# Kernel tuning notes

Hardware: AMD Instinct MI355X
Metric: run time of the kernel (lower is better)

## Reference

```python
import jax, jax.numpy as jnp
import numpy as np

N = 100000
E = 1600000
D = 128
EPS = 1e-5


def setup_inputs() -> dict:
    key = jax.random.key(0)
    ks = jax.random.split(key, 6)
    X = jax.random.normal(ks[0], (N, D), dtype=jnp.float32)
    edge_weight = jax.random.uniform(ks[1], (E,), dtype=jnp.float32)
    W = jax.random.normal(ks[2], (2 * D, D), dtype=jnp.float32) * (1.0 / np.sqrt(2 * D))
    b = jax.random.normal(ks[3], (D,), dtype=jnp.float32) * 0.01
    gamma = jnp.ones((D,), dtype=jnp.float32)
    beta = jnp.zeros((D,), dtype=jnp.float32)
    edge_src = jax.random.randint(ks[4], (E,), 0, N, dtype=jnp.int32)
    edge_dst = jax.random.randint(ks[5], (E,), 0, N, dtype=jnp.int32)
    return {"X": X, "edge_weight": edge_weight, "W": W, "b": b,
            "gamma": gamma, "beta": beta,
            "edge_src": edge_src, "edge_dst": edge_dst}


def reference(X, edge_weight, W, b, gamma, beta, edge_src, edge_dst):
    # Pre-LayerNorm over feature dim
    mu = jnp.mean(X, axis=-1, keepdims=True)
    var = jnp.mean(jnp.square(X - mu), axis=-1, keepdims=True)
    H = (X - mu) * jax.lax.rsqrt(var + EPS) * gamma + beta
    # dropout is identity in eval mode
    # sparse neighbor aggregation: neigh[i] = sum_{e: dst[e]=i} w[e] * H[src[e]]
    msgs = edge_weight[:, None] * H[edge_src]          # [E, D]
    neigh = jax.ops.segment_sum(msgs, edge_dst, num_segments=X.shape[0])  # [N, D]
    cat = jnp.concatenate([H, neigh], axis=1)          # [N, 2D]
    out = cat @ W + b                                  # [N, D]
    out = jax.nn.relu(out)
    return out + X                                     # residual (in_dim == out_dim)
```

## Files before the change

kernel.cpp:

```cpp
#include <hip/hip_runtime.h>
#include <hip/hip_bf16.h>

#define N_NODES 100000
#define D 128
#define E_EDGES 1600000

#define BSHIFT 6
#define BROWS 64
#define NBUCK 1563
#define CAP 1536
#define NBLK_S 256
#define SBLK 1024
#define EPB (E_EDGES / NBLK_S)
#define LN_BLOCKS ((N_NODES + 15) / 16)

typedef __attribute__((ext_vector_type(8))) short bf16x8;
typedef __attribute__((ext_vector_type(8))) unsigned short ushort8;
typedef __attribute__((ext_vector_type(4))) float f32x4;

__device__ __forceinline__ float bf2f(unsigned short u) {
    unsigned int x = ((unsigned int)u) << 16;
    return __builtin_bit_cast(float, x);
}
__device__ __forceinline__ unsigned short f2bf(float f) {
    unsigned int x = __builtin_bit_cast(unsigned int, f);
    unsigned int lsb = (x >> 16) & 1u;
    x += 0x7fffu + lsb;
    return (unsigned short)(x >> 16);
}

__global__ __launch_bounds__(256) void wt_kernel(
    const float* __restrict__ W, unsigned short* __restrict__ Wt)
{
    int i = blockIdx.x * 1024 + threadIdx.x * 4;
    #pragma unroll
    for (int j = 0; j < 4; ++j) {
        int idx = i + j;
        int k = idx >> 7, col = idx & 127;
        Wt[col * 256 + k] = f2bf(W[idx]);
    }
}

__global__ __launch_bounds__(1024) void fused_ln_scatter(
    const float* __restrict__ X,
    const float* __restrict__ gamma,
    const float* __restrict__ beta,
    unsigned short* __restrict__ H,
    const int* __restrict__ esrc, const int* __restrict__ edst,
    const float* __restrict__ ew,
    unsigned int* __restrict__ gcur,
    uint2* __restrict__ bins)
{
    __shared__ unsigned int h[NBUCK];

    if (blockIdx.x < NBLK_S) {
        const int t = threadIdx.x;
        for (int i = t; i < NBUCK; i += SBLK) h[i] = 0;
        __syncthreads();

        const int base = blockIdx.x * EPB;
        for (int k = t; k < EPB; k += SBLK)
            atomicAdd(&h[edst[base + k] >> BSHIFT], 1u);
        __syncthreads();

        for (int i = t; i < NBUCK; i += SBLK) {
            unsigned int c = h[i];
            h[i] = c ? atomicAdd(&gcur[i], c) : 0u;
        }
        __syncthreads();

        for (int k = t; k < EPB; k += SBLK) {
            int e = base + k;
            int d = edst[e];
            int bkt = d >> BSHIFT;
            unsigned int p = atomicAdd(&h[bkt], 1u);
            if (p < CAP)
                bins[(size_t)bkt * CAP + p] =
                    make_uint2((unsigned int)esrc[e] |
                               ((unsigned int)(d & (BROWS - 1)) << 17),
                               __builtin_bit_cast(unsigned int, ew[e]));
        }
    } else {
        int wid  = (blockIdx.x - NBLK_S) * (SBLK / 64) + (threadIdx.x >> 6);
        int lane = threadIdx.x & 63;
        if (wid >= N_NODES) return;

        const float2 x2 = *reinterpret_cast<const float2*>(X + (size_t)wid * D + 2 * lane);
        float x0 = x2.x, x1 = x2.y;
        float s  = x0 + x1;
        float sq = x0 * x0 + x1 * x1;
        #pragma unroll
        for (int m = 1; m < 64; m <<= 1) {
            s  += __shfl_xor(s,  m);
            sq += __shfl_xor(sq, m);
        }
        float mu   = s * (1.0f / 128.0f);
        float var  = sq * (1.0f / 128.0f) - mu * mu;
        float rstd = rsqrtf(var + 1e-5f);

        const float2 g2 = *reinterpret_cast<const float2*>(gamma + 2 * lane);
        const float2 b2 = *reinterpret_cast<const float2*>(beta  + 2 * lane);

        ushort2 h2;
        h2.x = f2bf((x0 - mu) * rstd * g2.x + b2.x);
        h2.y = f2bf((x1 - mu) * rstd * g2.y + b2.y);
        *reinterpret_cast<ushort2*>(H + (size_t)wid * D + 2 * lane) = h2;
    }
}

__global__ __launch_bounds__(256) void bucket_sort(
    uint2* __restrict__ bins,
    const unsigned int* __restrict__ gcur,
    uint2* __restrict__ offs2)
{
    __shared__ uint2 ent[CAP];
    __shared__ unsigned int cnt[BROWS];
    __shared__ unsigned int cur[BROWS];

    const int b = blockIdx.x;
    const int t = threadIdx.x;
    const unsigned int e0 = (unsigned int)b * CAP;
    const int nE = (int)min(gcur[b], (unsigned int)CAP);

    if (t < BROWS) cnt[t] = 0;
    __syncthreads();

    for (int k = t; k < nE; k += 256) {
        uint2 r = bins[e0 + k];
        ent[k] = r;
        atomicAdd(&cnt[r.x >> 17], 1u);
    }
    __syncthreads();

    if (t < BROWS) {
        unsigned int v = cnt[t], inc = v;
        #pragma unroll
        for (int off = 1; off < BROWS; off <<= 1) {
            unsigned int u = __shfl_up(inc, off);
            if (t >= off) inc += u;
        }
        unsigned int start = e0 + inc - v;
        cur[t] = start;
        int node = b * BROWS + t;
        if (node < N_NODES) offs2[node] = make_uint2(start, start + v);
    }
    __syncthreads();

    for (int k = t; k < nE; k += 256) {
        uint2 r = ent[k];
        unsigned int p = atomicAdd(&cur[r.x >> 17], 1u);
        bins[p] = make_uint2(r.x & 0x1FFFFu, r.y);
    }
}

__global__ __launch_bounds__(256) void aggregate_kernel(
    const unsigned short* __restrict__ H,
    const uint2* __restrict__ bins,
    const uint2* __restrict__ offs2,
    unsigned short* __restrict__ nb)
{
    int wid  = (blockIdx.x * blockDim.x + threadIdx.x) >> 6;
    int lane = threadIdx.x & 63;
    if (wid >= N_NODES) return;
    const int quarter = lane >> 4;
    const int l15     = lane & 15;

    const uint2 o = offs2[wid];
    const unsigned int e = o.x;
    const int n = (int)(o.y - o.x);

    float a0 = 0.f, a1 = 0.f, a2 = 0.f, a3 = 0.f;
    float a4 = 0.f, a5 = 0.f, a6 = 0.f, a7 = 0.f;

    int k = 0;
    for (; k + 8 <= n; k += 8) {
        uint2 r0 = bins[e + k + quarter];
        uint2 r1 = bins[e + k + 4 + quarter];
        ushort8 h0 = *reinterpret_cast<const ushort8*>(H + (size_t)r0.x * D + 8 * l15);
        ushort8 h1 = *reinterpret_cast<const ushort8*>(H + (size_t)r1.x * D + 8 * l15);
        float w0 = __builtin_bit_cast(float, r0.y);
        float w1 = __builtin_bit_cast(float, r1.y);
        a0 += w0 * bf2f(h0[0]) + w1 * bf2f(h1[0]);
        a1 += w0 * bf2f(h0[1]) + w1 * bf2f(h1[1]);
        a2 += w0 * bf2f(h0[2]) + w1 * bf2f(h1[2]);
        a3 += w0 * bf2f(h0[3]) + w1 * bf2f(h1[3]);
        a4 += w0 * bf2f(h0[4]) + w1 * bf2f(h1[4]);
        a5 += w0 * bf2f(h0[5]) + w1 * bf2f(h1[5]);
        a6 += w0 * bf2f(h0[6]) + w1 * bf2f(h1[6]);
        a7 += w0 * bf2f(h0[7]) + w1 * bf2f(h1[7]);
    }
    if (k + 4 <= n) {
        uint2 r0 = bins[e + k + quarter];
        ushort8 h0 = *reinterpret_cast<const ushort8*>(H + (size_t)r0.x * D + 8 * l15);
        float w0 = __builtin_bit_cast(float, r0.y);
        a0 += w0 * bf2f(h0[0]); a1 += w0 * bf2f(h0[1]);
        a2 += w0 * bf2f(h0[2]); a3 += w0 * bf2f(h0[3]);
        a4 += w0 * bf2f(h0[4]); a5 += w0 * bf2f(h0[5]);
        a6 += w0 * bf2f(h0[6]); a7 += w0 * bf2f(h0[7]);
        k += 4;
    }
    if (k < n) {
        bool valid = (k + quarter) < n;
        uint2 r0 = bins[valid ? (e + k + quarter) : e];
        ushort8 h0 = *reinterpret_cast<const ushort8*>(H + (size_t)r0.x * D + 8 * l15);
        float w0 = valid ? __builtin_bit_cast(float, r0.y) : 0.f;
        a0 += w0 * bf2f(h0[0]); a1 += w0 * bf2f(h0[1]);
        a2 += w0 * bf2f(h0[2]); a3 += w0 * bf2f(h0[3]);
        a4 += w0 * bf2f(h0[4]); a5 += w0 * bf2f(h0[5]);
        a6 += w0 * bf2f(h0[6]); a7 += w0 * bf2f(h0[7]);
    }

    a0 += __shfl_xor(a0, 16); a0 += __shfl_xor(a0, 32);
    a1 += __shfl_xor(a1, 16); a1 += __shfl_xor(a1, 32);
    a2 += __shfl_xor(a2, 16); a2 += __shfl_xor(a2, 32);
    a3 += __shfl_xor(a3, 16); a3 += __shfl_xor(a3, 32);
    a4 += __shfl_xor(a4, 16); a4 += __shfl_xor(a4, 32);
    a5 += __shfl_xor(a5, 16); a5 += __shfl_xor(a5, 32);
    a6 += __shfl_xor(a6, 16); a6 += __shfl_xor(a6, 32);
    a7 += __shfl_xor(a7, 16); a7 += __shfl_xor(a7, 32);

    if (quarter == 0) {
        ushort8 ov;
        ov[0] = f2bf(a0); ov[1] = f2bf(a1); ov[2] = f2bf(a2); ov[3] = f2bf(a3);
        ov[4] = f2bf(a4); ov[5] = f2bf(a5); ov[6] = f2bf(a6); ov[7] = f2bf(a7);
        *reinterpret_cast<ushort8*>(nb + (size_t)wid * D + 8 * l15) = ov;
    }
}

#define ROWS_PER_BLOCK 128
#define STRIPS 8

__global__ __launch_bounds__(256) void gemm_kernel(
    const unsigned short* __restrict__ H,
    const unsigned short* __restrict__ nb,
    const unsigned short* __restrict__ Wt,
    const float* __restrict__ bias,
    const float* __restrict__ X,
    float* __restrict__ out)
{
    __shared__ unsigned short lds[16][256];

    const int tid  = threadIdx.x;
    const int w    = tid >> 6;
    const int lane = tid & 63;
    const int l15  = lane & 15;
    const int l4   = lane >> 4;

    bf16x8 bfrag[2][8];
    #pragma unroll
    for (int t = 0; t < 2; ++t) {
        const int col = 32 * w + 16 * t + l15;
        #pragma unroll
        for (int s = 0; s < 8; ++s)
            bfrag[t][s] = *reinterpret_cast<const bf16x8*>(
                Wt + (size_t)col * 256 + 32 * s + 8 * l4);
    }
    const float bias0 = bias[32 * w + l15];
    const float bias1 = bias[32 * w + 16 + l15];

    const int row0_blk = blockIdx.x * ROWS_PER_BLOCK;

    for (int strip = 0; strip < STRIPS; ++strip) {
        const int r0 = row0_blk + strip * 16;
        __syncthreads();

        {
            const int row  = tid >> 4;
            const int c8   = tid & 15;
            const int grow = r0 + row;
            char* ldsrow = (char*)&lds[row][0];
            const int key = (row & 7) << 4;

            uint4 hv = make_uint4(0u, 0u, 0u, 0u);
            uint4 nv = make_uint4(0u, 0u, 0u, 0u);
            if (grow < N_NODES) {
                hv = *reinterpret_cast<const uint4*>(H  + (size_t)grow * D + 8 * c8);
                nv = *reinterpret_cast<const uint4*>(nb + (size_t)grow * D + 8 * c8);
            }
            *reinterpret_cast<uint4*>(ldsrow + ((16 * c8) ^ key)) = hv;
            *reinterpret_cast<uint4*>(ldsrow + ((256 + 16 * c8) ^ key)) = nv;
        }
        __syncthreads();

        f32x4 acc0 = {0.f, 0.f, 0.f, 0.f};
        f32x4 acc1 = {0.f, 0.f, 0.f, 0.f};
        const char* ldsa = (const char*)&lds[l15][0];
        const int   akey = (l15 & 7) << 4;
        #pragma unroll
        for (int s = 0; s < 8; ++s) {
            bf16x8 afrag = *reinterpret_cast<const bf16x8*>(
                ldsa + ((64 * s + 16 * l4) ^ akey));
            acc0 = __builtin_amdgcn_mfma_f32_16x16x32_bf16(afrag, bfrag[0][s], acc0, 0, 0, 0);
            acc1 = __builtin_amdgcn_mfma_f32_16x16x32_bf16(afrag, bfrag[1][s], acc1, 0, 0, 0);
        }

        #pragma unroll
        for (int r = 0; r < 4; ++r) {
            const int grow = r0 + 4 * l4 + r;
            if (grow < N_NODES) {
                const size_t base = (size_t)grow * D;
                const int c0 = 32 * w + l15;
                float v0 = acc0[r] + bias0;
                v0 = v0 > 0.f ? v0 : 0.f;
                out[base + c0] = v0 + X[base + c0];
                const int c1 = c0 + 16;
                float v1 = acc1[r] + bias1;
                v1 = v1 > 0.f ? v1 : 0.f;
                out[base + c1] = v1 + X[base + c1];
            }
        }
    }
}

extern "C" void kernel_launch(void* const* d_in, const int* in_sizes, int n_in,
                              void* d_out, int out_size, void* d_ws, size_t ws_size,
                              hipStream_t stream)
{
    const float* X     = (const float*)d_in[0];
    const float* ew    = (const float*)d_in[1];
    const float* W     = (const float*)d_in[2];
    const float* b     = (const float*)d_in[3];
    const float* gamma = (const float*)d_in[4];
    const float* beta  = (const float*)d_in[5];
    const int* esrc = (const int*)d_in[6];
    const int* edst = (const int*)d_in[7];
    float* out = (float*)d_out;

    unsigned short* H  = (unsigned short*)d_ws;
    unsigned short* nb = H + (size_t)N_NODES * D;
    uint2* bins = (uint2*)(nb + (size_t)N_NODES * D);
    unsigned int* gcur = (unsigned int*)(bins + (size_t)NBUCK * CAP);
    uint2* offs2 = (uint2*)(gcur + NBUCK + 1);
    unsigned short* Wt = (unsigned short*)(offs2 + N_NODES);

    hipMemsetAsync(gcur, 0, NBUCK * sizeof(unsigned int), stream);
    wt_kernel<<<32, 256, 0, stream>>>(W, Wt);
    fused_ln_scatter<<<NBLK_S + LN_BLOCKS, SBLK, 0, stream>>>(
        X, gamma, beta, H, esrc, edst, ew, gcur, bins);
    bucket_sort<<<NBUCK, 256, 0, stream>>>(bins, gcur, offs2);
    aggregate_kernel<<<(N_NODES + 3) / 4, 256, 0, stream>>>(H, bins, offs2, nb);
    gemm_kernel<<<(N_NODES + ROWS_PER_BLOCK - 1) / ROWS_PER_BLOCK, 256, 0, stream>>>(
        H, nb, Wt, b, X, out);
}
```

Measured before the change: 154.0 us.

## Fuse bucket sort and neighbor aggregation into one kernel using LDS-sorted edges

Merges the bucket_sort and aggregate kernels so each block counting-sorts its 64-node bucket into shared memory and then aggregates those nodes directly from LDS. This removes one kernel launch, the global write-back of sorted bins, the offs2 array, and the re-read of edges from global memory in the aggregate pass. In exchange, each block now runs 4 waves over 16 nodes each sequentially, which lowers parallelism and latency hiding for the H gathers compared with one wave per node across many blocks.

Result: faster. 147.3 us (-4.3%).

```diff
diff --git a/kernel.cpp b/kernel.cpp
--- a/kernel.cpp
+++ b/kernel.cpp
@@ -108,28 +108,27 @@
     }
 }
 
-__global__ __launch_bounds__(256) void bucket_sort(
-    uint2* __restrict__ bins,
+__global__ __launch_bounds__(256) void sort_aggregate(
+    const unsigned short* __restrict__ H,
+    const uint2* __restrict__ bins,
     const unsigned int* __restrict__ gcur,
-    uint2* __restrict__ offs2)
-{
-    __shared__ uint2 ent[CAP];
+    unsigned short* __restrict__ nb)
+{
+    __shared__ uint2 srt[CAP];
     __shared__ unsigned int cnt[BROWS];
     __shared__ unsigned int cur[BROWS];
+    __shared__ unsigned int starts[BROWS + 1];
 
     const int b = blockIdx.x;
     const int t = threadIdx.x;
-    const unsigned int e0 = (unsigned int)b * CAP;
+    const unsigned int gbase = (unsigned int)b * CAP;
     const int nE = (int)min(gcur[b], (unsigned int)CAP);
 
     if (t < BROWS) cnt[t] = 0;
     __syncthreads();
 
-    for (int k = t; k < nE; k += 256) {
-        uint2 r = bins[e0 + k];
-        ent[k] = r;
-        atomicAdd(&cnt[r.x >> 17], 1u);
-    }
+    for (int k = t; k < nE; k += 256)
+        atomicAdd(&cnt[bins[gbase + k].x >> 17], 1u);
     __syncthreads();
 
     if (t < BROWS) {
@@ -139,91 +138,88 @@
             unsigned int u = __shfl_up(inc, off);
             if (t >= off) inc += u;
         }
-        unsigned int start = e0 + inc - v;
+        unsigned int start = inc - v;
+        starts[t] = start;
         cur[t] = start;
-        int node = b * BROWS + t;
-        if (node < N_NODES) offs2[node] = make_uint2(start, start + v);
+        if (t == BROWS - 1) starts[BROWS] = inc;
     }
     __syncthreads();
 
     for (int k = t; k < nE; k += 256) {
-        uint2 r = ent[k];
+        uint2 r = bins[gbase + k];
         unsigned int p = atomicAdd(&cur[r.x >> 17], 1u);
-        bins[p] = make_uint2(r.x & 0x1FFFFu, r.y);
-    }
-}
-
-__global__ __launch_bounds__(256) void aggregate_kernel(
-    const unsigned short* __restrict__ H,
-    const uint2* __restrict__ bins,
-    const uint2* __restrict__ offs2,
-    unsigned short* __restrict__ nb)
-{
-    int wid  = (blockIdx.x * blockDim.x + threadIdx.x) >> 6;
-    int lane = threadIdx.x & 63;
-    if (wid >= N_NODES) return;
+        srt[p] = make_uint2(r.x & 0x1FFFFu, r.y);
+    }
+    __syncthreads();
+
+    const int wv      = t >> 6;
+    const int lane    = t & 63;
     const int quarter = lane >> 4;
     const int l15     = lane & 15;
 
-    const uint2 o = offs2[wid];
-    const unsigned int e = o.x;
-    const int n = (int)(o.y - o.x);
-
-    float a0 = 0.f, a1 = 0.f, a2 = 0.f, a3 = 0.f;
-    float a4 = 0.f, a5 = 0.f, a6 = 0.f, a7 = 0.f;
-
-    int k = 0;
-    for (; k + 8 <= n; k += 8) {
-        uint2 r0 = bins[e + k + quarter];
-        uint2 r1 = bins[e + k + 4 + quarter];
-        ushort8 h0 = *reinterpret_cast<const ushort8*>(H + (size_t)r0.x * D + 8 * l15);
-        ushort8 h1 = *reinterpret_cast<const ushort8*>(H + (size_t)r1.x * D + 8 * l15);
-        float w0 = __builtin_bit_cast(float, r0.y);
-        float w1 = __builtin_bit_cast(float, r1.y);
-        a0 += w0 * bf2f(h0[0]) + w1 * bf2f(h1[0]);
-        a1 += w0 * bf2f(h0[1]) + w1 * bf2f(h1[1]);
-        a2 += w0 * bf2f(h0[2]) + w1 * bf2f(h1[2]);
-        a3 += w0 * bf2f(h0[3]) + w1 * bf2f(h1[3]);
-        a4 += w0 * bf2f(h0[4]) + w1 * bf2f(h1[4]);
-        a5 += w0 * bf2f(h0[5]) + w1 * bf2f(h1[5]);
-        a6 += w0 * bf2f(h0[6]) + w1 * bf2f(h1[6]);
-        a7 += w0 * bf2f(h0[7]) + w1 * bf2f(h1[7]);
-    }
-    if (k + 4 <= n) {
-        uint2 r0 = bins[e + k + quarter];
-        ushort8 h0 = *reinterpret_cast<const ushort8*>(H + (size_t)r0.x * D + 8 * l15);
-        float w0 = __builtin_bit_cast(float, r0.y);
-        a0 += w0 * bf2f(h0[0]); a1 += w0 * bf2f(h0[1]);
-        a2 += w0 * bf2f(h0[2]); a3 += w0 * bf2f(h0[3]);
-        a4 += w0 * bf2f(h0[4]); a5 += w0 * bf2f(h0[5]);
-        a6 += w0 * bf2f(h0[6]); a7 += w0 * bf2f(h0[7]);
-        k += 4;
-    }
-    if (k < n) {
-        bool valid = (k + quarter) < n;
-        uint2 r0 = bins[valid ? (e + k + quarter) : e];
-        ushort8 h0 = *reinterpret_cast<const ushort8*>(H + (size_t)r0.x * D + 8 * l15);
-        float w0 = valid ? __builtin_bit_cast(float, r0.y) : 0.f;
-        a0 += w0 * bf2f(h0[0]); a1 += w0 * bf2f(h0[1]);
-        a2 += w0 * bf2f(h0[2]); a3 += w0 * bf2f(h0[3]);
-        a4 += w0 * bf2f(h0[4]); a5 += w0 * bf2f(h0[5]);
-        a6 += w0 * bf2f(h0[6]); a7 += w0 * bf2f(h0[7]);
-    }
-
-    a0 += __shfl_xor(a0, 16); a0 += __shfl_xor(a0, 32);
-    a1 += __shfl_xor(a1, 16); a1 += __shfl_xor(a1, 32);
-    a2 += __shfl_xor(a2, 16); a2 += __shfl_xor(a2, 32);
-    a3 += __shfl_xor(a3, 16); a3 += __shfl_xor(a3, 32);
-    a4 += __shfl_xor(a4, 16); a4 += __shfl_xor(a4, 32);
-    a5 += __shfl_xor(a5, 16); a5 += __shfl_xor(a5, 32);
-    a6 += __shfl_xor(a6, 16); a6 += __shfl_xor(a6, 32);
-    a7 += __shfl_xor(a7, 16); a7 += __shfl_xor(a7, 32);
-
-    if (quarter == 0) {
-        ushort8 ov;
-        ov[0] = f2bf(a0); ov[1] = f2bf(a1); ov[2] = f2bf(a2); ov[3] = f2bf(a3);
-        ov[4] = f2bf(a4); ov[5] = f2bf(a5); ov[6] = f2bf(a6); ov[7] = f2bf(a7);
-        *reinterpret_cast<ushort8*>(nb + (size_t)wid * D + 8 * l15) = ov;
+    for (int j = 0; j < 16; ++j) {
+        const int nl   = wv * 16 + j;
+        const int node = b * BROWS + nl;
+        if (node >= N_NODES) break;
+        const int s = (int)starts[nl];
+        const int n = (int)starts[nl + 1] - s;
+
+        float a0 = 0.f, a1 = 0.f, a2 = 0.f, a3 = 0.f;
+        float a4 = 0.f, a5 = 0.f, a6 = 0.f, a7 = 0.f;
+
+        int k = 0;
+        for (; k + 8 <= n; k += 8) {
+            uint2 r0 = srt[s + k + quarter];
+            uint2 r1 = srt[s + k + 4 + quarter];
+            ushort8 h0 = *reinterpret_cast<const ushort8*>(H + (size_t)r0.x * D + 8 * l15);
+            ushort8 h1 = *reinterpret_cast<const ushort8*>(H + (size_t)r1.x * D + 8 * l15);
+            float w0 = __builtin_bit_cast(float, r0.y);
+            float w1 = __builtin_bit_cast(float, r1.y);
+            a0 += w0 * bf2f(h0[0]) + w1 * bf2f(h1[0]);
+            a1 += w0 * bf2f(h0[1]) + w1 * bf2f(h1[1]);
+            a2 += w0 * bf2f(h0[2]) + w1 * bf2f(h1[2]);
+            a3 += w0 * bf2f(h0[3]) + w1 * bf2f(h1[3]);
+            a4 += w0 * bf2f(h0[4]) + w1 * bf2f(h1[4]);
+            a5 += w0 * bf2f(h0[5]) + w1 * bf2f(h1[5]);
+            a6 += w0 * bf2f(h0[6]) + w1 * bf2f(h1[6]);
+            a7 += w0 * bf2f(h0[7]) + w1 * bf2f(h1[7]);
+        }
+        if (k + 4 <= n) {
+            uint2 r0 = srt[s + k + quarter];
+            ushort8 h0 = *reinterpret_cast<const ushort8*>(H + (size_t)r0.x * D + 8 * l15);
+            float w0 = __builtin_bit_cast(float, r0.y);
+            a0 += w0 * bf2f(h0[0]); a1 += w0 * bf2f(h0[1]);
+            a2 += w0 * bf2f(h0[2]); a3 += w0 * bf2f(h0[3]);
+            a4 += w0 * bf2f(h0[4]); a5 += w0 * bf2f(h0[5]);
+            a6 += w0 * bf2f(h0[6]); a7 += w0 * bf2f(h0[7]);
+            k += 4;
+        }
+        if (k < n) {
+            bool valid = (k + quarter) < n;
+            uint2 r0 = srt[valid ? (s + k + quarter) : s];
+            ushort8 h0 = *reinterpret_cast<const ushort8*>(H + (size_t)r0.x * D + 8 * l15);
+            float w0 = valid ? __builtin_bit_cast(float, r0.y) : 0.f;
+            a0 += w0 * bf2f(h0[0]); a1 += w0 * bf2f(h0[1]);
+            a2 += w0 * bf2f(h0[2]); a3 += w0 * bf2f(h0[3]);
+            a4 += w0 * bf2f(h0[4]); a5 += w0 * bf2f(h0[5]);
+            a6 += w0 * bf2f(h0[6]); a7 += w0 * bf2f(h0[7]);
+        }
+
+        a0 += __shfl_xor(a0, 16); a0 += __shfl_xor(a0, 32);
+        a1 += __shfl_xor(a1, 16); a1 += __shfl_xor(a1, 32);
+        a2 += __shfl_xor(a2, 16); a2 += __shfl_xor(a2, 32);
+        a3 += __shfl_xor(a3, 16); a3 += __shfl_xor(a3, 32);
+        a4 += __shfl_xor(a4, 16); a4 += __shfl_xor(a4, 32);
+        a5 += __shfl_xor(a5, 16); a5 += __shfl_xor(a5, 32);
+        a6 += __shfl_xor(a6, 16); a6 += __shfl_xor(a6, 32);
+        a7 += __shfl_xor(a7, 16); a7 += __shfl_xor(a7, 32);
+
+        if (quarter == 0) {
+            ushort8 ov;
+            ov[0] = f2bf(a0); ov[1] = f2bf(a1); ov[2] = f2bf(a2); ov[3] = f2bf(a3);
+            ov[4] = f2bf(a4); ov[5] = f2bf(a5); ov[6] = f2bf(a6); ov[7] = f2bf(a7);
+            *reinterpret_cast<ushort8*>(nb + (size_t)node * D + 8 * l15) = ov;
+        }
     }
 }
 
@@ -330,15 +326,13 @@
     unsigned short* nb = H + (size_t)N_NODES * D;
     uint2* bins = (uint2*)(nb + (size_t)N_NODES * D);
     unsigned int* gcur = (unsigned int*)(bins + (size_t)NBUCK * CAP);
-    uint2* offs2 = (uint2*)(gcur + NBUCK + 1);
-    unsigned short* Wt = (unsigned short*)(offs2 + N_NODES);
+    unsigned short* Wt = (unsigned short*)(gcur + NBUCK + 1);
 
     hipMemsetAsync(gcur, 0, NBUCK * sizeof(unsigned int), stream);
     wt_kernel<<<32, 256, 0, stream>>>(W, Wt);
     fused_ln_scatter<<<NBLK_S + LN_BLOCKS, SBLK, 0, stream>>>(
         X, gamma, beta, H, esrc, edst, ew, gcur, bins);
-    bucket_sort<<<NBUCK, 256, 0, stream>>>(bins, gcur, offs2);
-    aggregate_kernel<<<(N_NODES + 3) / 4, 256, 0, stream>>>(H, bins, offs2, nb);
+    sort_aggregate<<<NBUCK, 256, 0, stream>>>(H, bins, gcur, nb);
     gemm_kernel<<<(N_NODES + ROWS_PER_BLOCK - 1) / ROWS_PER_BLOCK, 256, 0, stream>>>(
         H, nb, Wt, b, X, out);
 }
```
